# Optimization experiments

Measured on AMD Instinct MI355X. Metric: run time of the kernel, lower is better.

The kernel has to match this reference:

```python
import jax, jax.numpy as jnp
import numpy as np

Q_DIM = 256; KV_DIM = 256; C = 32; N_HEAD = 8; OUT_DIM = 256
B1, B2, LQ, LK = 1, 128, 256, 256


def _glorot(key, shape, gain=1.0):
    fan_in, fan_out = shape[-2], shape[-1]
    std = gain * np.sqrt(2.0 / float(fan_in + fan_out))
    dev = np.sqrt(3.0) * std
    return jax.random.uniform(key, shape, jnp.float32, -dev, dev)


def setup_inputs() -> dict:
    key = jax.random.key(0)
    ks = jax.random.split(key, 12)
    q_data = jax.random.normal(ks[0], (B1, B2, LQ, Q_DIM), jnp.float32)
    kv_data = jax.random.normal(ks[1], (B1, B2, LK, KV_DIM), jnp.float32)
    bias = jax.random.normal(ks[2], (B1, B2, N_HEAD, LQ, LK), jnp.float32)
    nonbatched_bias = jax.random.normal(ks[3], (B1, N_HEAD, LQ, LK), jnp.float32)
    # torch Linear weights are [out, in]; original init is zeros but we use
    # glorot for a non-degenerate numerical baseline.
    Wq = _glorot(ks[4], (N_HEAD * C, Q_DIM))
    Wk = _glorot(ks[5], (N_HEAD * C, KV_DIM))
    Wv = _glorot(ks[6], (N_HEAD * C, KV_DIM))
    Wg = _glorot(ks[7], (N_HEAD * C, Q_DIM))
    bg = jnp.ones((N_HEAD * C,), jnp.float32)  # bias_init=1.0
    Wo = _glorot(ks[8], (OUT_DIM, N_HEAD * C))
    bo = jnp.zeros((OUT_DIM,), jnp.float32)
    return dict(q_data=q_data, kv_data=kv_data, bias=bias,
                nonbatched_bias=nonbatched_bias, Wq=Wq, Wk=Wk, Wv=Wv,
                Wg=Wg, bg=bg, Wo=Wo, bo=bo)


def reference(q_data, kv_data, bias, nonbatched_bias, Wq, Wk, Wv, Wg, bg, Wo, bo):
    c = C
    # projections: [b1,b2,len,n_head,c]
    q = (q_data @ Wq.T).reshape(*q_data.shape[:-1], N_HEAD, c) * (c ** -0.5)
    k = (kv_data @ Wk.T).reshape(*kv_data.shape[:-1], N_HEAD, c)
    v = (kv_data @ Wv.T).reshape(*kv_data.shape[:-1], N_HEAD, c)
    # logits: [b1,b2,n_head,len_q,len_kv]
    logits = jnp.einsum('bsqhc,bskhc->bshqk', q, k)
    logits = logits + bias + nonbatched_bias[:, None]
    weights = jax.nn.softmax(logits, axis=-1)
    weighted_avg = jnp.einsum('bshqk,bskhc->bsqhc', weights, v)
    gate = jax.nn.sigmoid((q_data @ Wg.T + bg).reshape(*q_data.shape[:-1], N_HEAD, c))
    weighted_avg = weighted_avg * gate
    out = weighted_avg.reshape(*weighted_avg.shape[:-2], N_HEAD * c) @ Wo.T + bo
    return out
```

## Files before the change

kernel.cpp:

```cpp
#include <hip/hip_runtime.h>
#include <hip/hip_bf16.h>

#define NB2 128
#define LQK 256
#define DIM 256
#define NH 8
#define CC 32

typedef __bf16 bf16x8 __attribute__((ext_vector_type(8)));
typedef __bf16 bf16x4 __attribute__((ext_vector_type(4)));
typedef float f32x4 __attribute__((ext_vector_type(4)));

#define MFMA16 __builtin_amdgcn_mfma_f32_16x16x32_bf16

#define TP 72

#define NTOK ((size_t)NB2 * LQK * NH * CC)

static __device__ __forceinline__ void gload_lds16(const void* g, void* l) {
    __builtin_amdgcn_global_load_lds(
        (const __attribute__((address_space(1))) unsigned int*)g,
        (__attribute__((address_space(3))) unsigned int*)l,
        16, 0, 0);
}

__global__ __launch_bounds__(256) void k_cvt(
    const float* __restrict__ qd, const float* __restrict__ kvd,
    const float* __restrict__ Wq, const float* __restrict__ Wk,
    const float* __restrict__ Wv, const float* __restrict__ Wg,
    const float* __restrict__ Wo,
    __bf16* __restrict__ qbf, __bf16* __restrict__ kvbf,
    __bf16* __restrict__ wBF)
{
    const int b = blockIdx.x;
    if (b < 8192) {
        size_t i = ((size_t)b * 256 + threadIdx.x) * 8;
        const float* src;
        __bf16* dst;
        if (i < NTOK) { src = qd + i; dst = qbf + i; }
        else          { src = kvd + (i - NTOK); dst = kvbf + (i - NTOK); }
        f32x4 a = *(const f32x4*)src;
        f32x4 c = *(const f32x4*)(src + 4);
        bf16x8 r;
        r[0] = (__bf16)a[0]; r[1] = (__bf16)a[1]; r[2] = (__bf16)a[2]; r[3] = (__bf16)a[3];
        r[4] = (__bf16)c[0]; r[5] = (__bf16)c[1]; r[6] = (__bf16)c[2]; r[7] = (__bf16)c[3];
        *(bf16x8*)dst = r;
    } else {
        int i = ((b - 8192) * 256 + threadIdx.x) * 4;
        int mat = i >> 16;
        int off = i & 65535;
        const float* src = (mat == 0) ? Wq : (mat == 1) ? Wk : (mat == 2) ? Wv
                          : (mat == 3) ? Wg : Wo;
        f32x4 v = *(const f32x4*)(src + off);
        __bf16* d = wBF + ((size_t)mat << 16) + off;
        d[0] = (__bf16)v[0]; d[1] = (__bf16)v[1]; d[2] = (__bf16)v[2]; d[3] = (__bf16)v[3];
    }
}

__global__ __launch_bounds__(256, 2) void k_proj(
    const __bf16* __restrict__ qbf, const __bf16* __restrict__ kvbf,
    const __bf16* __restrict__ wBF, const float* __restrict__ bg,
    __bf16* __restrict__ wsq, __bf16* __restrict__ wsk,
    __bf16* __restrict__ wsvT, __bf16* __restrict__ wsgT)
{
    __shared__ __bf16 At[2][128][TP];
    __shared__ __bf16 Bt[2][128][TP];

    const int mb = blockIdx.x, nb = blockIdx.y;
    const int t = nb >> 1;
    const __bf16* X = (t == 0 || t == 3) ? qbf : kvbf;
    const __bf16* W = wBF + ((size_t)t << 16) + (size_t)((nb & 1) * 128) * 256;

    const int tid = threadIdx.x;
    const int lane = tid & 63, w = tid >> 6;
    const int g = lane >> 4, kg = g * 8, c0 = lane & 15;
    const int mq = (w >> 1) * 64, nq = (w & 1) * 64;
    const int m0 = mb * 128;
    const int srow = tid >> 1, shalf = (tid & 1) * 32;

    f32x4 acc[4][4] = {};
    bf16x8 av[4], bv[4];
    auto load_stage = [&](int kit) {
        const __bf16* ap = X + (size_t)(m0 + srow) * DIM + kit * 64 + shalf;
        const __bf16* bp = W + (size_t)srow * 256 + kit * 64 + shalf;
#pragma unroll
        for (int j = 0; j < 4; j++) {
            av[j] = *(const bf16x8*)(ap + j * 8);
            bv[j] = *(const bf16x8*)(bp + j * 8);
        }
    };
    auto write_stage = [&](int buf) {
#pragma unroll
        for (int j = 0; j < 4; j++) {
            *(bf16x8*)(&At[buf][srow][shalf + j * 8]) = av[j];
            *(bf16x8*)(&Bt[buf][srow][shalf + j * 8]) = bv[j];
        }
    };

    load_stage(0);
    write_stage(0);
    __syncthreads();

#pragma unroll
    for (int kit = 0; kit < 4; kit++) {
        if (kit < 3) load_stage(kit + 1);
        const int cur = kit & 1;
#pragma unroll
        for (int ks = 0; ks < 2; ks++) {
            bf16x8 af[4], bf_[4];
#pragma unroll
            for (int mi = 0; mi < 4; mi++)
                af[mi] = *(const bf16x8*)(&At[cur][mq + mi * 16 + c0][ks * 32 + kg]);
#pragma unroll
            for (int ni = 0; ni < 4; ni++)
                bf_[ni] = *(const bf16x8*)(&Bt[cur][nq + ni * 16 + c0][ks * 32 + kg]);
#pragma unroll
            for (int mi = 0; mi < 4; mi++)
#pragma unroll
                for (int ni = 0; ni < 4; ni++)
                    acc[mi][ni] = MFMA16(af[mi], bf_[ni], acc[mi][ni], 0, 0, 0);
        }
        if (kit < 3) write_stage(cur ^ 1);
        __syncthreads();
    }

#pragma unroll
    for (int ni = 0; ni < 4; ni++) {
        const int nloc = (nb & 1) * 128 + nq + ni * 16 + c0;
        const int h = nloc >> 5, c = nloc & 31;
        const float bg_ = (t == 3) ? bg[nloc] : 0.0f;
#pragma unroll
        for (int mi = 0; mi < 4; mi++) {
            const int mbase = m0 + mq + mi * 16 + g * 4;
            const int b2 = mbase >> 8;
            if (t == 2) {
                bf16x4 pk;
#pragma unroll
                for (int reg = 0; reg < 4; reg++) pk[reg] = (__bf16)acc[mi][ni][reg];
                *(bf16x4*)(&wsvT[((size_t)(b2 * NH + h) * CC + c) * LQK + (mbase & 255)]) = pk;
            } else if (t == 3) {
                bf16x4 pk;
#pragma unroll
                for (int reg = 0; reg < 4; reg++)
                    pk[reg] = (__bf16)(1.0f / (1.0f + __expf(-(acc[mi][ni][reg] + bg_))));
                *(bf16x4*)(&wsgT[((size_t)(b2 * NH + h) * CC + c) * LQK + (mbase & 255)]) = pk;
            } else {
#pragma unroll
                for (int reg = 0; reg < 4; reg++) {
                    const int l = (mbase + reg) & 255;
                    float v = acc[mi][ni][reg];
                    size_t idx = ((size_t)(b2 * NH + h) * LQK + l) * CC + c;
                    if (t == 0) wsq[idx] = (__bf16)(v * 0.17677669529663689f);
                    else        wsk[idx] = (__bf16)v;
                }
            }
        }
    }
}

__global__ __launch_bounds__(256, 3) void k_attn(
    const __bf16* __restrict__ wsq, const __bf16* __restrict__ wsk,
    const __bf16* __restrict__ wsvT, const __bf16* __restrict__ wsgT,
    const float* __restrict__ bias, const float* __restrict__ nbb,
    __bf16* __restrict__ wswa)
{
    __shared__ float  Bl[2][64][64];
    __shared__ __bf16 Kl[2][2048];
    __shared__ __bf16 P[4][16][TP];

    const int tid = threadIdx.x;
    const int u0 = blockIdx.x;
    const int xcd = u0 & 7, slot = u0 >> 3;
    const int head = xcd + 8 * (slot >> 2);
    const int qt = slot & 3;
    const int b2 = head >> 3, h = head & 7;

    const int lane = tid & 63, w = tid >> 6;
    const int g = lane >> 4, kg = g * 8, c0 = lane & 15;
    const int qbase = qt * 64 + w * 16;
    const int q = qbase + c0;
    const int rw = w * 16 + c0;

    const __bf16* qp = wsq + (size_t)(b2 * NH + h) * LQK * CC;
    const __bf16* kp = wsk + (size_t)(b2 * NH + h) * LQK * CC;
    const __bf16* vT = wsvT + (size_t)(b2 * NH + h) * CC * LQK;
    const __bf16* gT = wsgT + (size_t)(b2 * NH + h) * CC * LQK;
    const float* np = nbb + ((size_t)h * LQK + q) * LQK;
    const float* bblk = bias + ((size_t)(b2 * NH + h) * LQK + qt * 64) * LQK;

    auto stage = [&](int buf, int c) {
        const int rbase = tid >> 4, jj = tid & 15;
#pragma unroll
        for (int i = 0; i < 4; i++) {
            const int row = i * 16 + rbase;
            const int uu = jj ^ (row & 7);
            gload_lds16(bblk + (size_t)row * LQK + c * 64 + uu * 4,
                        &Bl[buf][i * 16 + w * 4][0]);
        }
        {
            const int su = (lane & 3) ^ ((lane >> 3) & 3);
            gload_lds16(kp + (size_t)(c * 64 + w * 16 + (lane >> 2)) * CC + su * 8,
                        &Kl[buf][w * 512]);
        }
    };

    bf16x8 qf = *(const bf16x8*)(qp + (size_t)q * CC + kg);

    stage(0, 0);
    __syncthreads();

    float l = 0.0f;
    f32x4 o[2] = {};

#pragma unroll
    for (int c = 0; c < 4; c++) {
        const int cur = c & 1;

        bf16x8 vf[4];
        f32x4 n4[4];
#pragma unroll
        for (int kt2 = 0; kt2 < 2; kt2++)
#pragma unroll
            for (int vn = 0; vn < 2; vn++)
                vf[kt2 * 2 + vn] = *(const bf16x8*)(
                    vT + (size_t)(vn * 16 + c0) * LQK + c * 64 + kt2 * 32 + kg);
#pragma unroll
        for (int j = 0; j < 4; j++)
            n4[j] = *(const f32x4*)(np + c * 64 + j * 16 + g * 4);
        __builtin_amdgcn_sched_barrier(0);

        if (c < 3) stage(cur ^ 1, c + 1);
        __builtin_amdgcn_sched_barrier(0);

        float csum = 0.0f;
#pragma unroll
        for (int j = 0; j < 4; j++) {
            const int su = ((j * 4 + g) ^ (rw & 7)) * 4;
            f32x4 b4 = *(const f32x4*)(&Bl[cur][rw][su]);
            bf16x8 kf = *(const bf16x8*)(
                &Kl[cur][((j * 16 + c0) * 4 + (g ^ ((c0 >> 1) & 3))) * 8]);
            f32x4 cc;
#pragma unroll
            for (int r2 = 0; r2 < 4; r2++) cc[r2] = b4[r2] + n4[j][r2];
            f32x4 s = MFMA16(kf, qf, cc, 0, 0, 0);
            bf16x4 pk;
#pragma unroll
            for (int r2 = 0; r2 < 4; r2++) {
                float e = __expf(s[r2]);
                csum += e;
                pk[r2] = (__bf16)e;
            }
            *(bf16x4*)(&P[w][c0][j * 16 + g * 4]) = pk;
        }
        l += csum;
#pragma unroll
        for (int kt2 = 0; kt2 < 2; kt2++) {
            bf16x8 pa = *(const bf16x8*)(&P[w][c0][kt2 * 32 + kg]);
#pragma unroll
            for (int vn = 0; vn < 2; vn++)
                o[vn] = MFMA16(pa, vf[kt2 * 2 + vn], o[vn], 0, 0, 0);
        }
        if (c < 3) __syncthreads();
    }

    l += __shfl_xor(l, 16);
    l += __shfl_xor(l, 32);
    const float inv = 1.0f / l;

#pragma unroll
    for (int vn = 0; vn < 2; vn++) {
        const int c = vn * 16 + c0;
        bf16x4 g4 = *(const bf16x4*)(gT + (size_t)c * LQK + qbase + g * 4);
#pragma unroll
        for (int reg = 0; reg < 4; reg++) {
            const int row = qbase + g * 4 + reg;
            const float invr = __shfl(inv, g * 4 + reg, 64);
            const float val = o[vn][reg] * invr * (float)g4[reg];
            wswa[((size_t)(b2 * LQK + row)) * (NH * CC) + h * CC + c] = (__bf16)val;
        }
    }
}

__global__ __launch_bounds__(256, 2) void k_out(
    const __bf16* __restrict__ wa, const __bf16* __restrict__ wBF,
    const float* __restrict__ bo, float* __restrict__ out)
{
    __shared__ __bf16 At[2][128][TP];
    __shared__ __bf16 Bt[2][128][TP];

    const int mb = blockIdx.x, nb = blockIdx.y;
    const __bf16* W = wBF + ((size_t)4 << 16) + (size_t)(nb * 128) * 256;

    const int tid = threadIdx.x;
    const int lane = tid & 63, w = tid >> 6;
    const int g = lane >> 4, kg = g * 8, c0 = lane & 15;
    const int mq = (w >> 1) * 64, nq = (w & 1) * 64;
    const int m0 = mb * 128;
    const int srow = tid >> 1, shalf = (tid & 1) * 32;

    f32x4 acc[4][4] = {};
    bf16x8 av[4], bv[4];
    auto load_stage = [&](int kit) {
        const __bf16* ap = wa + (size_t)(m0 + srow) * 256 + kit * 64 + shalf;
        const __bf16* bp = W + (size_t)srow * 256 + kit * 64 + shalf;
#pragma unroll
        for (int j = 0; j < 4; j++) {
            av[j] = *(const bf16x8*)(ap + j * 8);
            bv[j] = *(const bf16x8*)(bp + j * 8);
        }
    };
    auto write_stage = [&](int buf) {
#pragma unroll
        for (int j = 0; j < 4; j++) {
            *(bf16x8*)(&At[buf][srow][shalf + j * 8]) = av[j];
            *(bf16x8*)(&Bt[buf][srow][shalf + j * 8]) = bv[j];
        }
    };

    load_stage(0);
    write_stage(0);
    __syncthreads();

#pragma unroll
    for (int kit = 0; kit < 4; kit++) {
        if (kit < 3) load_stage(kit + 1);
        const int cur = kit & 1;
#pragma unroll
        for (int ks = 0; ks < 2; ks++) {
            bf16x8 af[4], bf_[4];
#pragma unroll
            for (int mi = 0; mi < 4; mi++)
                af[mi] = *(const bf16x8*)(&At[cur][mq + mi * 16 + c0][ks * 32 + kg]);
#pragma unroll
            for (int ni = 0; ni < 4; ni++)
                bf_[ni] = *(const bf16x8*)(&Bt[cur][nq + ni * 16 + c0][ks * 32 + kg]);
#pragma unroll
            for (int mi = 0; mi < 4; mi++)
#pragma unroll
                for (int ni = 0; ni < 4; ni++)
                    acc[mi][ni] = MFMA16(af[mi], bf_[ni], acc[mi][ni], 0, 0, 0);
        }
        if (kit < 3) write_stage(cur ^ 1);
        __syncthreads();
    }

#pragma unroll
    for (int ni = 0; ni < 4; ni++) {
        const int n = nb * 128 + nq + ni * 16 + c0;
        const float bo_ = bo[n];
#pragma unroll
        for (int mi = 0; mi < 4; mi++) {
            const int mbase = m0 + mq + mi * 16 + g * 4;
#pragma unroll
            for (int reg = 0; reg < 4; reg++)
                out[(size_t)(mbase + reg) * 256 + n] = acc[mi][ni][reg] + bo_;
        }
    }
}

extern "C" void kernel_launch(void* const* d_in, const int* in_sizes, int n_in,
                              void* d_out, int out_size, void* d_ws, size_t ws_size,
                              hipStream_t stream) {
    const float* qd  = (const float*)d_in[0];
    const float* kvd = (const float*)d_in[1];
    const float* bias = (const float*)d_in[2];
    const float* nbb = (const float*)d_in[3];
    const float* Wq = (const float*)d_in[4];
    const float* Wk = (const float*)d_in[5];
    const float* Wv = (const float*)d_in[6];
    const float* Wg = (const float*)d_in[7];
    const float* bg = (const float*)d_in[8];
    const float* Wo = (const float*)d_in[9];
    const float* bo = (const float*)d_in[10];
    float* out = (float*)d_out;

    __bf16* ws = (__bf16*)d_ws;
    __bf16* wsq  = ws;
    __bf16* wsk  = wsq + NTOK;
    __bf16* wsvT = wsk + NTOK;
    __bf16* wsgT = wsvT + NTOK;
    __bf16* wBF  = wsgT + NTOK;
    __bf16* qbf  = wBF + 5 * 65536;
    __bf16* kvbf = qbf + NTOK;
    __bf16* wswa = qbf;

    k_cvt<<<dim3(8512), 256, 0, stream>>>(qd, kvd, Wq, Wk, Wv, Wg, Wo,
                                          qbf, kvbf, wBF);
    k_proj<<<dim3(256, 8), 256, 0, stream>>>(qbf, kvbf, wBF, bg,
                                             wsq, wsk, wsvT, wsgT);
    k_attn<<<dim3(4096), 256, 0, stream>>>(wsq, wsk, wsvT, wsgT, bias, nbb, wswa);
    k_out<<<dim3(256, 2), 256, 0, stream>>>(wswa, wBF, bo, out);
}
```

Measured before the change: 168.5 us.

## Split attention keys across waves with cross-wave reduction of outputs

Changes the k_attn work split so each wave owns a 64-key slice, with its K and V held in registers, instead of owning 16 queries and streaming K chunks through LDS. The block now iterates over 16-query groups. Partial outputs and softmax row sums from the four waves are reduced through shared memory, then normalized and gated before the store. This removes K staging to LDS but adds two block barriers per step, LDS traffic for the partial outputs, and scalar gate loads and stores.

```diff
diff --git a/kernel.cpp b/kernel.cpp
--- a/kernel.cpp
+++ b/kernel.cpp
@@ -164,9 +164,10 @@
     const float* __restrict__ bias, const float* __restrict__ nbb,
     __bf16* __restrict__ wswa)
 {
-    __shared__ float  Bl[2][64][64];
-    __shared__ __bf16 Kl[2][2048];
+    __shared__ float  Bl[2][16][256];
     __shared__ __bf16 P[4][16][TP];
+    __shared__ float  lsum[4][16];
+    __shared__ float  op[4][16][33];
 
     const int tid = threadIdx.x;
     const int u0 = blockIdx.x;
@@ -177,72 +178,60 @@
 
     const int lane = tid & 63, w = tid >> 6;
     const int g = lane >> 4, kg = g * 8, c0 = lane & 15;
-    const int qbase = qt * 64 + w * 16;
-    const int q = qbase + c0;
-    const int rw = w * 16 + c0;
 
     const __bf16* qp = wsq + (size_t)(b2 * NH + h) * LQK * CC;
     const __bf16* kp = wsk + (size_t)(b2 * NH + h) * LQK * CC;
     const __bf16* vT = wsvT + (size_t)(b2 * NH + h) * CC * LQK;
     const __bf16* gT = wsgT + (size_t)(b2 * NH + h) * CC * LQK;
-    const float* np = nbb + ((size_t)h * LQK + q) * LQK;
+    const float* npb = nbb + (size_t)h * LQK * LQK;
     const float* bblk = bias + ((size_t)(b2 * NH + h) * LQK + qt * 64) * LQK;
 
-    auto stage = [&](int buf, int c) {
-        const int rbase = tid >> 4, jj = tid & 15;
+    auto stage = [&](int buf, int p) {
 #pragma unroll
         for (int i = 0; i < 4; i++) {
-            const int row = i * 16 + rbase;
-            const int uu = jj ^ (row & 7);
-            gload_lds16(bblk + (size_t)row * LQK + c * 64 + uu * 4,
-                        &Bl[buf][i * 16 + w * 4][0]);
-        }
-        {
-            const int su = (lane & 3) ^ ((lane >> 3) & 3);
-            gload_lds16(kp + (size_t)(c * 64 + w * 16 + (lane >> 2)) * CC + su * 8,
-                        &Kl[buf][w * 512]);
-        }
-    };
-
-    bf16x8 qf = *(const bf16x8*)(qp + (size_t)q * CC + kg);
+            const int row = w * 4 + i;
+            gload_lds16(bblk + (size_t)(p * 16 + row) * LQK + ((lane ^ row) * 4),
+                        &Bl[buf][row][0]);
+        }
+    };
+
+    bf16x8 kf[4], vf[4];
+#pragma unroll
+    for (int j = 0; j < 4; j++)
+        kf[j] = *(const bf16x8*)(kp + (size_t)(w * 64 + j * 16 + c0) * CC + kg);
+#pragma unroll
+    for (int kt2 = 0; kt2 < 2; kt2++)
+#pragma unroll
+        for (int vn = 0; vn < 2; vn++)
+            vf[kt2 * 2 + vn] = *(const bf16x8*)(
+                vT + (size_t)(vn * 16 + c0) * LQK + w * 64 + kt2 * 32 + kg);
 
     stage(0, 0);
     __syncthreads();
 
-    float l = 0.0f;
-    f32x4 o[2] = {};
-
-#pragma unroll
-    for (int c = 0; c < 4; c++) {
-        const int cur = c & 1;
-
-        bf16x8 vf[4];
-        f32x4 n4[4];
-#pragma unroll
-        for (int kt2 = 0; kt2 < 2; kt2++)
-#pragma unroll
-            for (int vn = 0; vn < 2; vn++)
-                vf[kt2 * 2 + vn] = *(const bf16x8*)(
-                    vT + (size_t)(vn * 16 + c0) * LQK + c * 64 + kt2 * 32 + kg);
+#pragma unroll
+    for (int p = 0; p < 4; p++) {
+        const int cur = p & 1;
+        const int qglob = qt * 64 + p * 16 + c0;
+
+        bf16x8 qf = *(const bf16x8*)(qp + (size_t)qglob * CC + kg);
+        f32x4 nb4[4];
 #pragma unroll
         for (int j = 0; j < 4; j++)
-            n4[j] = *(const f32x4*)(np + c * 64 + j * 16 + g * 4);
+            nb4[j] = *(const f32x4*)(npb + (size_t)qglob * LQK + w * 64 + j * 16 + g * 4);
         __builtin_amdgcn_sched_barrier(0);
 
-        if (c < 3) stage(cur ^ 1, c + 1);
+        if (p < 3) stage(cur ^ 1, p + 1);
         __builtin_amdgcn_sched_barrier(0);
 
         float csum = 0.0f;
 #pragma unroll
         for (int j = 0; j < 4; j++) {
-            const int su = ((j * 4 + g) ^ (rw & 7)) * 4;
-            f32x4 b4 = *(const f32x4*)(&Bl[cur][rw][su]);
-            bf16x8 kf = *(const bf16x8*)(
-                &Kl[cur][((j * 16 + c0) * 4 + (g ^ ((c0 >> 1) & 3))) * 8]);
+            f32x4 b4 = *(const f32x4*)(&Bl[cur][c0][(w * 16 + ((j * 4 + g) ^ c0)) * 4]);
             f32x4 cc;
 #pragma unroll
-            for (int r2 = 0; r2 < 4; r2++) cc[r2] = b4[r2] + n4[j][r2];
-            f32x4 s = MFMA16(kf, qf, cc, 0, 0, 0);
+            for (int r2 = 0; r2 < 4; r2++) cc[r2] = b4[r2] + nb4[j][r2];
+            f32x4 s = MFMA16(kf[j], qf, cc, 0, 0, 0);
             bf16x4 pk;
 #pragma unroll
             for (int r2 = 0; r2 < 4; r2++) {
@@ -252,32 +241,41 @@
             }
             *(bf16x4*)(&P[w][c0][j * 16 + g * 4]) = pk;
         }
-        l += csum;
+        csum += __shfl_xor(csum, 16);
+        csum += __shfl_xor(csum, 32);
+        if (lane < 16) lsum[w][lane] = csum;
+
+        f32x4 o2[2] = {};
 #pragma unroll
         for (int kt2 = 0; kt2 < 2; kt2++) {
             bf16x8 pa = *(const bf16x8*)(&P[w][c0][kt2 * 32 + kg]);
 #pragma unroll
             for (int vn = 0; vn < 2; vn++)
-                o[vn] = MFMA16(pa, vf[kt2 * 2 + vn], o[vn], 0, 0, 0);
-        }
-        if (c < 3) __syncthreads();
-    }
-
-    l += __shfl_xor(l, 16);
-    l += __shfl_xor(l, 32);
-    const float inv = 1.0f / l;
-
-#pragma unroll
-    for (int vn = 0; vn < 2; vn++) {
-        const int c = vn * 16 + c0;
-        bf16x4 g4 = *(const bf16x4*)(gT + (size_t)c * LQK + qbase + g * 4);
-#pragma unroll
-        for (int reg = 0; reg < 4; reg++) {
-            const int row = qbase + g * 4 + reg;
-            const float invr = __shfl(inv, g * 4 + reg, 64);
-            const float val = o[vn][reg] * invr * (float)g4[reg];
-            wswa[((size_t)(b2 * LQK + row)) * (NH * CC) + h * CC + c] = (__bf16)val;
-        }
+                o2[vn] = MFMA16(pa, vf[kt2 * 2 + vn], o2[vn], 0, 0, 0);
+        }
+#pragma unroll
+        for (int vn = 0; vn < 2; vn++)
+#pragma unroll
+            for (int r2 = 0; r2 < 4; r2++)
+                op[w][g * 4 + r2][vn * 16 + c0] = o2[vn][r2];
+
+        __syncthreads();
+
+        {
+            const int idx = tid * 2;
+            const int qr = idx >> 5;
+            const int cbase = idx & 31;
+            const int qg = qt * 64 + p * 16 + qr;
+            const float li = 1.0f / (lsum[0][qr] + lsum[1][qr] + lsum[2][qr] + lsum[3][qr]);
+#pragma unroll
+            for (int e = 0; e < 2; e++) {
+                const int cc2 = cbase + e;
+                float val = op[0][qr][cc2] + op[1][qr][cc2] + op[2][qr][cc2] + op[3][qr][cc2];
+                val *= li * (float)gT[(size_t)cc2 * LQK + qg];
+                wswa[((size_t)(b2 * LQK + qg)) * (NH * CC) + h * CC + cc2] = (__bf16)val;
+            }
+        }
+        __syncthreads();
     }
 }
 
```

Result: faster. 164.0 us (-2.6%).
